# Optimization experiments

Hardware: AMD Instinct MI355X
Metric: run time of the kernel (lower is better)

## Reference

```python
import jax, jax.numpy as jnp
import numpy as np

BOUND = np.array([[-4.0, 4.0], [-4.0, 4.0], [-2.0, 2.0]], dtype=np.float32)
N_PTS = 1048576
PLANE_C = 3
PLANE_RES = [128, 256, 512, 1024]
N_LEVELS = 16
F_PER = 2
T = 2 ** 16  # hashmap size (log2_hashmap_size=16)
BASE_RES = 16
FINEST = int(float((BOUND[:, 1] - BOUND[:, 0]).max()) / 0.02)  # 400
_growth = np.exp(np.log(FINEST / BASE_RES) / (N_LEVELS - 1))
HASH_RES = np.floor(BASE_RES * _growth ** np.arange(N_LEVELS)).astype(np.float32)
PRIMES = jnp.array([1, 2654435761, 805459861], dtype=jnp.uint32)


def setup_inputs() -> dict:
    key = jax.random.key(0)
    ks = jax.random.split(key, 32)
    lo = jnp.asarray(BOUND[:, 0]); hi = jnp.asarray(BOUND[:, 1])
    inp = {}
    inp['p'] = jax.random.uniform(ks[0], (N_PTS, 3), dtype=jnp.float32) * (hi - lo) + lo
    i = 1
    for li, r in enumerate(PLANE_RES):
        for name in ('xy', 'xz', 'yz'):
            inp[f'plane_{name}_{li}'] = 0.1 * jax.random.normal(ks[i], (PLANE_C, r, r), dtype=jnp.float32)
            i += 1
    inp['hash_table'] = jax.random.uniform(ks[i], (N_LEVELS, T, F_PER), dtype=jnp.float32, minval=-1e-4, maxval=1e-4); i += 1

    def lin(k, fi, fo):
        s = 1.0 / np.sqrt(fi)
        k1, k2 = jax.random.split(k)
        return (jax.random.uniform(k1, (fi, fo), minval=-s, maxval=s, dtype=jnp.float32),
                jax.random.uniform(k2, (fo,), minval=-s, maxval=s, dtype=jnp.float32))

    c_in = 12 * PLANE_C + N_LEVELS * F_PER  # 68
    inp['W0'], inp['b0'] = lin(ks[i], c_in, 64); i += 1
    inp['W1'], inp['b1'] = lin(ks[i], 64, 64); i += 1
    inp['Wo'], inp['bo'] = lin(ks[i], 64, 33); i += 1  # 1 sdf + 32 geo_feat
    inp['Wc0'], inp['bc0'] = lin(ks[i], 12 * PLANE_C + 32, 64); i += 1
    inp['Wc1'], inp['bc1'] = lin(ks[i], 64, 32); i += 1
    inp['Wco'], inp['bco'] = lin(ks[i], 32, 3); i += 1
    return inp


def sample_plane(plane, u, v):
    """Bilinear grid_sample, align_corners=True, padding_mode='border'.
    plane: (C,H,W); u indexes W, v indexes H; u,v in [-1,1]. Returns (N,C)."""
    C, H, W = plane.shape
    x = jnp.clip((u + 1.0) * 0.5 * (W - 1), 0.0, W - 1)
    y = jnp.clip((v + 1.0) * 0.5 * (H - 1), 0.0, H - 1)
    x0 = jnp.floor(x); y0 = jnp.floor(y)
    wx = x - x0; wy = y - y0
    x0i = x0.astype(jnp.int32); y0i = y0.astype(jnp.int32)
    x1i = jnp.minimum(x0i + 1, W - 1); y1i = jnp.minimum(y0i + 1, H - 1)
    g = lambda yi, xi: plane[:, yi, xi]  # (C,N)
    out = (g(y0i, x0i) * ((1 - wy) * (1 - wx)) + g(y0i, x1i) * ((1 - wy) * wx)
           + g(y1i, x0i) * (wy * (1 - wx)) + g(y1i, x1i) * (wy * wx))
    return out.T


def hash_encode(p01, table):
    """Multi-res hash grid (instant-ngp style). p01: (N,3) in [0,1]; table: (L,T,F) -> (N, L*F)."""
    res = jnp.asarray(HASH_RES)  # (L,)

    def level(r, tab):
        x = p01 * r
        x0 = jnp.floor(x)
        w = x - x0
        xi = x0.astype(jnp.uint32)  # (N,3)
        feat = jnp.zeros((p01.shape[0], F_PER), dtype=table.dtype)
        for dz in (0, 1):
            for dy in (0, 1):
                for dx in (0, 1):
                    c = xi + jnp.array([dx, dy, dz], dtype=jnp.uint32)
                    h = c * PRIMES[None, :]
                    idx = ((h[:, 0] ^ h[:, 1] ^ h[:, 2]) % T).astype(jnp.int32)
                    wgt = ((w[:, 0] if dx else 1 - w[:, 0])
                           * (w[:, 1] if dy else 1 - w[:, 1])
                           * (w[:, 2] if dz else 1 - w[:, 2]))
                    feat = feat + tab[idx] * wgt[:, None]
        return feat  # (N,F)

    feats = jax.vmap(level, in_axes=(0, 0))(res, table)  # (L,N,F)
    return jnp.transpose(feats, (1, 0, 2)).reshape(p01.shape[0], N_LEVELS * F_PER)


def _forward(p, plane_xy_0, plane_xz_0, plane_yz_0, plane_xy_1, plane_xz_1, plane_yz_1,
             plane_xy_2, plane_xz_2, plane_yz_2, plane_xy_3, plane_xz_3, plane_yz_3,
             hash_table, W0, b0, W1, b1, Wo, bo, Wc0, bc0, Wc1, bc1, Wco, bco):
    bound = jnp.asarray(BOUND)
    p_nor = (p - bound[:, 0]) / (bound[:, 1] - bound[:, 0]) * 2.0 - 1.0  # normalize_3d_coordinate
    u, v, w = p_nor[:, 0], p_nor[:, 1], p_nor[:, 2]
    levels = [(plane_xy_0, plane_xz_0, plane_yz_0), (plane_xy_1, plane_xz_1, plane_yz_1),
              (plane_xy_2, plane_xz_2, plane_yz_2), (plane_xy_3, plane_xz_3, plane_yz_3)]
    feats = []
    for pxy, pxz, pyz in levels:
        feats += [sample_plane(pxy, u, v), sample_plane(pxz, u, w), sample_plane(pyz, v, w)]
    plane_feat = jnp.concatenate(feats, axis=-1)  # (N, 36)
    hfeat = hash_encode((p_nor + 1.0) * 0.5, hash_table)  # (N, 32)
    # SDF branch
    h = jnp.concatenate([plane_feat, hfeat], axis=-1)  # (N, 68)
    h = jax.nn.relu(h @ W0 + b0)
    h = jax.nn.relu(h @ W1 + b1)
    sf = jnp.tanh(h @ Wo + bo)
    sdf, geo_feat = sf[:, :1], sf[:, 1:]
    # RGB branch
    c = jnp.concatenate([geo_feat, plane_feat], axis=-1)  # (N, 68)
    c = jax.nn.relu(c @ Wc0 + bc0)
    c = jax.nn.relu(c @ Wc1 + bc1)
    rgb = jax.nn.sigmoid(c @ Wco + bco)
    return jnp.concatenate([rgb, sdf], axis=-1)  # (N, 4)


def reference(p, plane_xy_0, plane_xz_0, plane_yz_0, plane_xy_1, plane_xz_1, plane_yz_1,
              plane_xy_2, plane_xz_2, plane_yz_2, plane_xy_3, plane_xz_3, plane_yz_3,
              hash_table, W0, b0, W1, b1, Wo, bo, Wc0, bc0, Wc1, bc1, Wco, bco):
    return _forward(p, plane_xy_0, plane_xz_0, plane_yz_0, plane_xy_1, plane_xz_1, plane_yz_1,
                    plane_xy_2, plane_xz_2, plane_yz_2, plane_xy_3, plane_xz_3, plane_yz_3,
                    hash_table, W0, b0, W1, b1, Wo, bo, Wc0, bc0, Wc1, bc1, Wco, bco)
```

## Files before the change

kernel.cpp:

```cpp
#include <hip/hip_runtime.h>

#define NPTS 1048576
#define NBKT 262144

typedef short bhalf8 __attribute__((ext_vector_type(8)));
typedef _Float16 halfv8 __attribute__((ext_vector_type(8)));
typedef _Float16 halfv2 __attribute__((ext_vector_type(2)));
typedef float floatx4 __attribute__((ext_vector_type(4)));

#define WSZ 24320
#define MLP_THREADS 1024
#define MLP_WAVES 16

#define PB_PLANES 16320
#define PB_HASH 4096
#define PB_HIST 4096

__device__ const float HRg[16] = {16.f, 19.f, 24.f, 30.f, 37.f, 46.f, 57.f, 71.f,
                                  89.f, 110.f, 136.f, 169.f, 210.f, 260.f, 322.f, 400.f};


__device__ __forceinline__ float my_tanh(float x) {
  float e = __expf(2.f * x);
  return 1.f - 2.f * __builtin_amdgcn_rcpf(e + 1.f);
}

__device__ __forceinline__ float my_sigmoid(float x) {
  return __builtin_amdgcn_rcpf(1.f + __expf(-x));
}

__device__ __forceinline__ unsigned short f2h(float v) {
  _Float16 h = (_Float16)v;
  unsigned short u;
  __builtin_memcpy(&u, &h, 2);
  return u;
}

__device__ __forceinline__ float h2f(unsigned short u) {
  _Float16 h;
  __builtin_memcpy(&h, &u, 2);
  return (float)h;
}

__device__ __forceinline__ float texch(uint2 t, int c) {
  unsigned short u = (c == 0) ? (unsigned short)(t.x & 0xffffu)
                   : (c == 1) ? (unsigned short)(t.x >> 16)
                              : (unsigned short)(t.y & 0xffffu);
  return h2f(u);
}

__device__ __forceinline__ unsigned mort6(unsigned x) {
  return (x & 1) | ((x & 2) << 2) | ((x & 4) << 4) |
         ((x & 8) << 6) | ((x & 16) << 8) | ((x & 32) << 10);
}

__device__ __forceinline__ unsigned morton_key(float px, float py, float pz) {
  float qx = (px + 4.f) * 0.125f, qy = (py + 4.f) * 0.125f, qz = (pz + 2.f) * 0.25f;
  unsigned kx = min(63, max(0, (int)(qx * 64.f)));
  unsigned ky = min(63, max(0, (int)(qy * 64.f)));
  unsigned kz = min(63, max(0, (int)(qz * 64.f)));
  return mort6(kx) | (mort6(ky) << 1) | (mort6(kz) << 2);
}

__device__ __forceinline__ unsigned hash_level(const unsigned* __restrict__ ht, int lv,
                                               float q0, float q1, float q2) {
  const float r = HRg[lv];
  float x0 = q0 * r, x1 = q1 * r, x2 = q2 * r;
  float f0 = floorf(x0), f1 = floorf(x1), f2 = floorf(x2);
  float w0 = x0 - f0, w1 = x1 - f1, w2 = x2 - f2;
  unsigned i0 = (unsigned)(int)f0, i1 = (unsigned)(int)f1, i2 = (unsigned)(int)f2;
  const unsigned* __restrict__ hb = ht + ((unsigned)lv << 16);
  unsigned tv[8];
#pragma unroll
  for (int dz = 0; dz < 2; ++dz)
#pragma unroll
    for (int dy = 0; dy < 2; ++dy)
#pragma unroll
      for (int dx = 0; dx < 2; ++dx) {
        unsigned h = (i0 + dx) ^ ((i1 + dy) * 2654435761u) ^ ((i2 + dz) * 805459861u);
        tv[dz * 4 + dy * 2 + dx] = hb[h & 65535u];
      }
  halfv2 acc2 = {(_Float16)0.f, (_Float16)0.f};
#pragma unroll
  for (int c = 0; c < 8; ++c) {
    const int dx = c & 1, dy = (c >> 1) & 1, dz = c >> 2;
    float wgt = (dx ? w0 : 1.f - w0) * (dy ? w1 : 1.f - w1) * (dz ? w2 : 1.f - w2);
    halfv2 th;
    __builtin_memcpy(&th, &tv[c], 4);
    _Float16 wh = (_Float16)wgt;
    halfv2 w2v = {wh, wh};
    acc2 = th * w2v + acc2;
  }
  unsigned res;
  __builtin_memcpy(&res, &acc2, 4);
  return res;
}

__device__ __forceinline__ uint2 sampleP(const uint2* __restrict__ planes, int s,
                                         float u, float v, float w) {
  const int level = s / 3;
  const int m = s - level * 3;
  const float a = (m == 2) ? v : u;
  const float b = (m == 0) ? v : w;
  const int R = 128 << level;
  const unsigned base = 16384u * ((1u << (2 * level)) - 1u) + (unsigned)m * (unsigned)(R * R);
  const float Rm1 = (float)(R - 1);
  float x = fminf(fmaxf((a + 1.f) * 0.5f * Rm1, 0.f), Rm1);
  float y = fminf(fmaxf((b + 1.f) * 0.5f * Rm1, 0.f), Rm1);
  float x0f = floorf(x), y0f = floorf(y);
  float wx = x - x0f, wy = y - y0f;
  int x0 = (int)x0f, y0 = (int)y0f;
  int x1 = min(x0 + 1, R - 1), y1 = min(y0 + 1, R - 1);
  uint2 t00 = planes[base + y0 * R + x0];
  uint2 t01 = planes[base + y0 * R + x1];
  uint2 t10 = planes[base + y1 * R + x0];
  uint2 t11 = planes[base + y1 * R + x1];
  _Float16 h00 = (_Float16)((1.f - wy) * (1.f - wx));
  _Float16 h01 = (_Float16)((1.f - wy) * wx);
  _Float16 h10 = (_Float16)(wy * (1.f - wx));
  _Float16 h11 = (_Float16)(wy * wx);
  halfv2 w00 = {h00, h00}, w01 = {h01, h01}, w10 = {h10, h10}, w11 = {h11, h11};
  halfv2 l00, l01, l10, l11, u00, u01, u10, u11;
  __builtin_memcpy(&l00, &t00.x, 4); __builtin_memcpy(&u00, &t00.y, 4);
  __builtin_memcpy(&l01, &t01.x, 4); __builtin_memcpy(&u01, &t01.y, 4);
  __builtin_memcpy(&l10, &t10.x, 4); __builtin_memcpy(&u10, &t10.y, 4);
  __builtin_memcpy(&l11, &t11.x, 4); __builtin_memcpy(&u11, &t11.y, 4);
  halfv2 alo = l00 * w00 + l01 * w01 + l10 * w10 + l11 * w11;
  halfv2 ahi = u00 * w00 + u01 * w01 + u10 * w10 + u11 * w11;
  uint2 r;
  __builtin_memcpy(&r.x, &alo, 4);
  __builtin_memcpy(&r.y, &ahi, 4);
  return r;
}


struct PrepParams {
  const float* psrc[12];
  ushort4* pdst[12];
  const float* hash;
  unsigned* hashb;
  const float* p;
  unsigned* hist;
};

__global__ __launch_bounds__(256) void prep_kernel(PrepParams P) {
  const int b = blockIdx.x;
  if (b < PB_PLANES) {
    const int CUM[13] = {0, 16384, 32768, 49152, 114688, 180224, 245760,
                         507904, 770048, 1032192, 2080768, 3129344, 4177920};
    const int RESL[12] = {128, 128, 128, 256, 256, 256, 512, 512, 512, 1024, 1024, 1024};
    const int s = b << 8;
    int pi = 0;
#pragma unroll
    for (int i = 1; i < 12; ++i)
      if (s >= CUM[i]) pi = i;
    const int li = s + threadIdx.x - CUM[pi];
    const int R = RESL[pi];
    const int n = R * R;
    const float* __restrict__ src = P.psrc[pi];
    ushort4 t;
    t.x = f2h(src[li]);
    t.y = f2h(src[n + li]);
    t.z = f2h(src[2 * n + li]);
    t.w = 0;
    P.pdst[pi][li] = t;
  } else if (b < PB_PLANES + PB_HASH) {
    const int i = ((b - PB_PLANES) << 8) + threadIdx.x;
    float2 v = *(const float2*)(P.hash + (size_t)i * 2);
    P.hashb[i] = (unsigned)f2h(v.x) | ((unsigned)f2h(v.y) << 16);
  } else {
    const int i = ((b - PB_PLANES - PB_HASH) << 8) + threadIdx.x;
    const float* pp = P.p + (size_t)i * 3;
    unsigned k = morton_key(pp[0], pp[1], pp[2]);
    atomicAdd(&P.hist[k], 1u);
  }
}


__global__ __launch_bounds__(256) void scan1_kernel(const unsigned* __restrict__ hist,
                                                    unsigned* __restrict__ partial) {
  __shared__ unsigned s[256];
  const int b = blockIdx.x, t = threadIdx.x;
  uint4 v = ((const uint4*)(hist + b * 1024))[t];
  s[t] = v.x + v.y + v.z + v.w;
  __syncthreads();
  for (int d = 128; d > 0; d >>= 1) {
    if (t < d) s[t] += s[t + d];
    __syncthreads();
  }
  if (t == 0) partial[b] = s[0];
}

__global__ __launch_bounds__(256) void scan2_kernel(const unsigned* __restrict__ partial,
                                                    unsigned* __restrict__ base) {
  __shared__ unsigned s[256];
  const int t = threadIdx.x;
  s[t] = partial[t];
  __syncthreads();
  for (int d = 1; d < 256; d <<= 1) {
    unsigned v = (t >= d) ? s[t - d] : 0u;
    __syncthreads();
    s[t] += v;
    __syncthreads();
  }
  base[t] = (t == 0) ? 0u : s[t - 1];
}

__global__ __launch_bounds__(256) void scan3_kernel(const unsigned* __restrict__ hist,
                                                    const unsigned* __restrict__ base,
                                                    unsigned* __restrict__ cursor) {
  __shared__ unsigned s[256];
  const int b = blockIdx.x, t = threadIdx.x;
  uint4 v = ((const uint4*)(hist + b * 1024))[t];
  unsigned sum = v.x + v.y + v.z + v.w;
  s[t] = sum;
  __syncthreads();
  for (int d = 1; d < 256; d <<= 1) {
    unsigned x = (t >= d) ? s[t - d] : 0u;
    __syncthreads();
    s[t] += x;
    __syncthreads();
  }
  unsigned off = base[b] + s[t] - sum;
  uint4 c;
  c.x = off;
  c.y = off + v.x;
  c.z = off + v.x + v.y;
  c.w = off + v.x + v.y + v.z;
  ((uint4*)(cursor + b * 1024))[t] = c;
}

__global__ __launch_bounds__(256) void scatter_kernel(const float* __restrict__ p,
                                                      unsigned* __restrict__ cursor,
                                                      float4* __restrict__ qs) {
  int i = blockIdx.x * 256 + threadIdx.x;
  const float* pp = p + (size_t)i * 3;
  const float px = pp[0], py = pp[1], pz = pp[2];
  unsigned k = morton_key(px, py, pz);
  unsigned slot = atomicAdd(&cursor[k], 1u);
  float4 q;
  q.x = (px + 4.f) * 0.125f;
  q.y = (py + 4.f) * 0.125f;
  q.z = (pz + 2.f) * 0.25f;
  q.w = __uint_as_float((unsigned)i);
  qs[slot] = q;
}


__global__ __launch_bounds__(256) void repack_plane(const float* __restrict__ src,
                                                    ushort4* __restrict__ dst, int R) {
  int i = blockIdx.x * 256 + threadIdx.x;
  int n = R * R;
  if (i >= n) return;
  ushort4 t;
  t.x = f2h(src[i]);
  t.y = f2h(src[n + i]);
  t.z = f2h(src[2 * n + i]);
  t.w = 0;
  dst[i] = t;
}


__device__ __forceinline__ void sample3i(const uint2* __restrict__ pl,
                                         float a, float b, int R, float* f) {
  const float Rm1 = (float)(R - 1);
  float x = fminf(fmaxf((a + 1.f) * 0.5f * Rm1, 0.f), Rm1);
  float y = fminf(fmaxf((b + 1.f) * 0.5f * Rm1, 0.f), Rm1);
  float x0f = floorf(x), y0f = floorf(y);
  float wx = x - x0f, wy = y - y0f;
  int x0 = (int)x0f, y0 = (int)y0f;
  int x1 = min(x0 + 1, R - 1), y1 = min(y0 + 1, R - 1);
  float w00 = (1.f - wy) * (1.f - wx);
  float w01 = (1.f - wy) * wx;
  float w10 = wy * (1.f - wx);
  float w11 = wy * wx;
  uint2 t00 = pl[y0 * R + x0];
  uint2 t01 = pl[y0 * R + x1];
  uint2 t10 = pl[y1 * R + x0];
  uint2 t11 = pl[y1 * R + x1];
#pragma unroll
  for (int c = 0; c < 3; ++c) {
    f[c] = texch(t00, c) * w00 + texch(t01, c) * w01 +
           texch(t10, c) * w10 + texch(t11, c) * w11;
  }
}

__device__ __forceinline__ void sample3f(const float* __restrict__ pl,
                                         float a, float b, int R, float* f) {
  const float Rm1 = (float)(R - 1);
  float x = fminf(fmaxf((a + 1.f) * 0.5f * Rm1, 0.f), Rm1);
  float y = fminf(fmaxf((b + 1.f) * 0.5f * Rm1, 0.f), Rm1);
  float x0f = floorf(x), y0f = floorf(y);
  float wx = x - x0f, wy = y - y0f;
  int x0 = (int)x0f, y0 = (int)y0f;
  int x1 = min(x0 + 1, R - 1), y1 = min(y0 + 1, R - 1);
  float w00 = (1.f - wy) * (1.f - wx);
  float w01 = (1.f - wy) * wx;
  float w10 = wy * (1.f - wx);
  float w11 = wy * wx;
  int i00 = y0 * R + x0, i01 = y0 * R + x1;
  int i10 = y1 * R + x0, i11 = y1 * R + x1;
  const int R2 = R * R;
#pragma unroll
  for (int c = 0; c < 3; ++c) {
    const float* base = pl + c * R2;
    f[c] = base[i00] * w00 + base[i01] * w01 + base[i10] * w10 + base[i11] * w11;
  }
}


struct MlpWParams {
  const uint2* planes;
  const unsigned* hashb;
  const float4* qs;
  const float* W0; const float* b0;
  const float* W1; const float* b1;
  const float* Wo; const float* bo;
  const float* Wc0; const float* bc0;
  const float* Wc1; const float* bc1;
  const float* Wco; const float* bco;
  float* out;
};

template <int MODE>
__device__ __forceinline__ void stage_w(const float* __restrict__ src, int K, int Nsrc,
                                        int STR, int NPAD, int OFF, short* Wlds, int tid) {
  const int total = NPAD * STR;
  for (int idx = tid; idx < total; idx += MLP_THREADS) {
    int c = idx / STR;
    int kp = idx - c * STR;
    int sk = -1;
    if (MODE == 0) {
      if (kp < 48) {
        int s = kp >> 2, ch = kp & 3;
        if (ch < 3) sk = s * 3 + ch;
      } else if (kp < 80) {
        sk = 36 + (kp - 48);
      }
    } else if (MODE == 1) {
      if (kp < 32) {
        sk = kp;
      } else if (kp < 80) {
        int s = (kp - 32) >> 2, ch = (kp - 32) & 3;
        if (ch < 3) sk = 32 + s * 3 + ch;
      }
    } else {
      if (kp < K) sk = kp;
    }
    float val = (sk >= 0 && c < Nsrc) ? src[sk * Nsrc + c] : 0.f;
    Wlds[OFF + idx] = (short)f2h(val);
  }
}

__device__ __forceinline__ void stage_b(const float* __restrict__ src, int Nsrc, int NPAD,
                                        int BOFF, float* Blds, int tid) {
  for (int j = tid; j < NPAD; j += MLP_THREADS) Blds[BOFF + j] = (j < Nsrc) ? src[j] : 0.f;
}

__device__ __forceinline__ halfv8 as_h8(bhalf8 s) {
  halfv8 h;
  __builtin_memcpy(&h, &s, 16);
  return h;
}

__device__ __forceinline__ halfv8 frag4(unsigned d0, unsigned d1, unsigned d2, unsigned d3) {
  bhalf8 r;
  r[0] = (short)(d0 & 0xffffu); r[1] = (short)(d0 >> 16);
  r[2] = (short)(d1 & 0xffffu); r[3] = (short)(d1 >> 16);
  r[4] = (short)(d2 & 0xffffu); r[5] = (short)(d2 >> 16);
  r[6] = (short)(d3 & 0xffffu); r[7] = (short)(d3 >> 16);
  return as_h8(r);
}

__device__ __forceinline__ halfv8 ldS(const short* scr, int rowl, int grp, int s) {
  return *(const halfv8*)&scr[rowl * 72 + 32 * s + 8 * grp];
}

template <int NT, int KS, int OFF, int STR>
__device__ __forceinline__ void mlayer(const halfv8 (&af)[KS], floatx4 (&acc)[NT],
                                       const short* Wlds, int rowl, int grp) {
#pragma unroll
  for (int n = 0; n < NT; ++n) {
    floatx4 a{};
#pragma unroll
    for (int s = 0; s < KS; ++s) {
      const int wo = OFF + (16 * n + rowl) * STR + 32 * s + 8 * grp;
      const halfv8 wA = *(const halfv8*)&Wlds[wo];
      a = __builtin_amdgcn_mfma_f32_16x16x32_f16(wA, af[s], a, 0, 0, 0);
    }
    acc[n] = a;
  }
}

template <int NT>
__device__ __forceinline__ void relu_wr(const floatx4 (&acc)[NT], const float* Blds,
                                        int boff, short* scr, int rowl, int grp) {
#pragma unroll
  for (int n = 0; n < NT; ++n) {
    const int cbase = 16 * n + 4 * grp;
    short4 v4;
    float v0 = fmaxf(acc[n][0] + Blds[boff + cbase + 0], 0.f);
    float v1 = fmaxf(acc[n][1] + Blds[boff + cbase + 1], 0.f);
    float v2 = fmaxf(acc[n][2] + Blds[boff + cbase + 2], 0.f);
    float v3 = fmaxf(acc[n][3] + Blds[boff + cbase + 3], 0.f);
    v4.x = (short)f2h(v0);
    v4.y = (short)f2h(v1);
    v4.z = (short)f2h(v2);
    v4.w = (short)f2h(v3);
    *(short4*)&scr[rowl * 72 + cbase] = v4;
  }
}

__device__ __forceinline__ void tanh_wr(const floatx4 (&acc)[3], const float* Blds,
                                        short* scr, float* ost, int rowl, int grp) {
#pragma unroll
  for (int n = 0; n < 3; ++n) {
#pragma unroll
    for (int r = 0; r < 4; ++r) {
      const int c = 16 * n + 4 * grp + r;
      float v = my_tanh(acc[n][r] + Blds[128 + c]);
      if (c == 0) ost[rowl * 4 + 3] = v;
      if (c >= 1 && c <= 32) scr[rowl * 72 + c - 1] = (short)f2h(v);
    }
  }
}

__global__ __launch_bounds__(MLP_THREADS) void mlp_fused(MlpWParams P) {
  __shared__ short Wlds[WSZ];
  __shared__ float Blds[288];
  __shared__ short Scr[MLP_WAVES * 16 * 72];
  __shared__ float Ost[MLP_WAVES][16][4];

  const int tid = threadIdx.x;

  stage_w<0>(P.W0,  96, 64, 104, 64,     0, Wlds, tid);
  stage_w<2>(P.W1,  64, 64,  72, 64,  6656, Wlds, tid);
  stage_w<2>(P.Wo,  64, 33,  72, 48, 11264, Wlds, tid);
  stage_w<1>(P.Wc0, 96, 64, 104, 64, 14720, Wlds, tid);
  stage_w<2>(P.Wc1, 64, 32,  72, 32, 21376, Wlds, tid);
  stage_w<2>(P.Wco, 32,  3,  40, 16, 23680, Wlds, tid);
  stage_b(P.b0,  64, 64,   0, Blds, tid);
  stage_b(P.b1,  64, 64,  64, Blds, tid);
  stage_b(P.bo,  33, 48, 128, Blds, tid);
  stage_b(P.bc0, 64, 64, 176, Blds, tid);
  stage_b(P.bc1, 32, 32, 240, Blds, tid);
  stage_b(P.bco,  3, 16, 272, Blds, tid);
  __syncthreads();

  const int wave = tid >> 6, lane = tid & 63;
  const int rowl = lane & 15, grp = lane >> 4;
  short* scr0 = &Scr[wave * 16 * 72];
  float* ost0 = &Ost[wave][0][0];

  int bid = blockIdx.x;
  bid = (bid & 7) * 64 + (bid >> 3);

  for (int t = 0; t < 8; ++t) {
    const int wbase = ((bid * 8 + t) * MLP_WAVES + wave) * 16;
    const int pt = wbase + rowl;

    float4 q4 = P.qs[pt];
    const float q0 = q4.x, q1 = q4.y, q2 = q4.z;
    const unsigned pid = __float_as_uint(q4.w);
    const float u = 2.f * q0 - 1.f;
    const float v = 2.f * q1 - 1.f;
    const float w = 2.f * q2 - 1.f;

    uint2 sA = sampleP(P.planes, 2 * grp, u, v, w);
    uint2 sB = sampleP(P.planes, 2 * grp + 1, u, v, w);
    uint2 sC = {0u, 0u}, sD = {0u, 0u};
    if (grp < 2) {
      sC = sampleP(P.planes, 8 + 2 * grp, u, v, w);
      sD = sampleP(P.planes, 9 + 2 * grp, u, v, w);
    }
    const int lbase = (grp < 2) ? (8 + 4 * grp) : (4 * grp - 8);
    unsigned h0 = hash_level(P.hashb, lbase + 0, q0, q1, q2);
    unsigned h1 = hash_level(P.hashb, lbase + 1, q0, q1, q2);
    unsigned h2 = hash_level(P.hashb, lbase + 2, q0, q1, q2);
    unsigned h3 = hash_level(P.hashb, lbase + 3, q0, q1, q2);

    halfv8 af0 = frag4(sA.x, sA.y, sB.x, sB.y);
    halfv8 af1 = (grp < 2) ? frag4(sC.x, sC.y, sD.x, sD.y) : frag4(h0, h1, h2, h3);
    halfv8 af2 = (grp < 2) ? frag4(h0, h1, h2, h3) : frag4(0u, 0u, 0u, 0u);
    halfv8 zf = frag4(0u, 0u, 0u, 0u);

    {
      halfv8 afA[3] = {af0, af1, af2};
      floatx4 accA[4];
      mlayer<4, 3, 0, 104>(afA, accA, Wlds, rowl, grp);
      relu_wr<4>(accA, Blds, 0, scr0, rowl, grp);
    }
    {
      halfv8 afA[2] = {ldS(scr0, rowl, grp, 0), ldS(scr0, rowl, grp, 1)};
      floatx4 accA[4];
      mlayer<4, 2, 6656, 72>(afA, accA, Wlds, rowl, grp);
      relu_wr<4>(accA, Blds, 64, scr0, rowl, grp);
    }
    {
      halfv8 afA[2] = {ldS(scr0, rowl, grp, 0), ldS(scr0, rowl, grp, 1)};
      floatx4 accA[3];
      mlayer<3, 2, 11264, 72>(afA, accA, Wlds, rowl, grp);
      tanh_wr(accA, Blds, scr0, ost0, rowl, grp);
    }
    {
      halfv8 afA[3] = {ldS(scr0, rowl, grp, 0), af0, (grp < 2) ? af1 : zf};
      floatx4 accA[4];
      mlayer<4, 3, 14720, 104>(afA, accA, Wlds, rowl, grp);
      relu_wr<4>(accA, Blds, 176, scr0, rowl, grp);
    }
    {
      halfv8 afA[2] = {ldS(scr0, rowl, grp, 0), ldS(scr0, rowl, grp, 1)};
      floatx4 accA[2];
      mlayer<2, 2, 21376, 72>(afA, accA, Wlds, rowl, grp);
      relu_wr<2>(accA, Blds, 240, scr0, rowl, grp);
    }
    {
      halfv8 afA[1] = {ldS(scr0, rowl, grp, 0)};
      floatx4 accA[1];
      mlayer<1, 1, 23680, 40>(afA, accA, Wlds, rowl, grp);
#pragma unroll
      for (int r = 0; r < 4; ++r) {
        const int c = 4 * grp + r;
        if (c < 3) {
          float vA = my_sigmoid(accA[0][r] + Blds[272 + c]);
          ost0[rowl * 4 + c] = vA;
        }
      }
    }

    if (lane < 16) {
      float4 o = *(float4*)&Ost[wave][lane][0];
      ((float4*)P.out)[pid] = o;
    }
  }
}


struct DecParams {
  const float* p;
  const float* pl[12];
  const uint2* pli[12];
  const float* hash;
  const float* W0; const float* b0;
  const float* W1; const float* b1;
  const float* Wo; const float* bo;
  const float* Wc0; const float* bc0;
  const float* Wc1; const float* bc1;
  const float* Wco; const float* bco;
  float* out;
};

template <bool ILV>
__global__ __launch_bounds__(256) void dec_kernel(DecParams P) {
  const int tid = blockIdx.x * 256 + threadIdx.x;

  const float* __restrict__ pp = P.p + (size_t)tid * 3;
  const float px = pp[0], py = pp[1], pz = pp[2];

  const float u = (px + 4.f) * 0.25f - 1.f;
  const float v = (py + 4.f) * 0.25f - 1.f;
  const float w = (pz + 2.f) * 0.5f - 1.f;

  float feat[68];
  {
    const int RES[4] = {128, 256, 512, 1024};
#pragma unroll
    for (int li = 0; li < 4; ++li) {
      if (ILV) {
        sample3i(P.pli[li * 3 + 0], u, v, RES[li], &feat[li * 9 + 0]);
        sample3i(P.pli[li * 3 + 1], u, w, RES[li], &feat[li * 9 + 3]);
        sample3i(P.pli[li * 3 + 2], v, w, RES[li], &feat[li * 9 + 6]);
      } else {
        sample3f(P.pl[li * 3 + 0], u, v, RES[li], &feat[li * 9 + 0]);
        sample3f(P.pl[li * 3 + 1], u, w, RES[li], &feat[li * 9 + 3]);
        sample3f(P.pl[li * 3 + 2], v, w, RES[li], &feat[li * 9 + 6]);
      }
    }
  }

  {
    const float q0 = (px + 4.f) * 0.125f;
    const float q1 = (py + 4.f) * 0.125f;
    const float q2 = (pz + 2.f) * 0.25f;
    const float* __restrict__ ht = P.hash;
#pragma unroll
    for (int l = 0; l < 16; ++l) {
      const float r = HRg[l];
      float x0 = q0 * r, x1 = q1 * r, x2 = q2 * r;
      float f0 = floorf(x0), f1 = floorf(x1), f2 = floorf(x2);
      float w0 = x0 - f0, w1 = x1 - f1, w2 = x2 - f2;
      unsigned i0 = (unsigned)(int)f0, i1 = (unsigned)(int)f1, i2 = (unsigned)(int)f2;
      float a0 = 0.f, a1 = 0.f;
#pragma unroll
      for (int dz = 0; dz < 2; ++dz)
#pragma unroll
        for (int dy = 0; dy < 2; ++dy)
#pragma unroll
          for (int dx = 0; dx < 2; ++dx) {
            unsigned h = (i0 + dx) ^ ((i1 + dy) * 2654435761u) ^ ((i2 + dz) * 805459861u);
            unsigned idx = h & 65535u;
            const float2 tv = *(const float2*)(ht + (((unsigned)l << 16) + idx) * 2);
            float wgt = (dx ? w0 : 1.f - w0) * (dy ? w1 : 1.f - w1) * (dz ? w2 : 1.f - w2);
            a0 = fmaf(tv.x, wgt, a0);
            a1 = fmaf(tv.y, wgt, a1);
          }
      feat[36 + l * 2] = a0;
      feat[36 + l * 2 + 1] = a1;
    }
  }

  float acc[64];
#pragma unroll
  for (int j = 0; j < 64; ++j) acc[j] = P.b0[j];
#pragma unroll
  for (int i = 0; i < 68; ++i) {
    const float a = feat[i];
    const float* wr = P.W0 + i * 64;
#pragma unroll
    for (int j = 0; j < 64; ++j) acc[j] = fmaf(a, wr[j], acc[j]);
  }
  float hid[64];
#pragma unroll
  for (int j = 0; j < 64; ++j) hid[j] = fmaxf(acc[j], 0.f);

#pragma unroll
  for (int j = 0; j < 64; ++j) acc[j] = P.b1[j];
#pragma unroll
  for (int i = 0; i < 64; ++i) {
    const float a = hid[i];
    const float* wr = P.W1 + i * 64;
#pragma unroll
    for (int j = 0; j < 64; ++j) acc[j] = fmaf(a, wr[j], acc[j]);
  }
#pragma unroll
  for (int j = 0; j < 64; ++j) hid[j] = fmaxf(acc[j], 0.f);

  float so[33];
#pragma unroll
  for (int j = 0; j < 33; ++j) so[j] = P.bo[j];
#pragma unroll
  for (int i = 0; i < 64; ++i) {
    const float a = hid[i];
    const float* wr = P.Wo + i * 33;
#pragma unroll
    for (int j = 0; j < 33; ++j) so[j] = fmaf(a, wr[j], so[j]);
  }
  const float sdf = my_tanh(so[0]);
  float geo[32];
#pragma unroll
  for (int j = 0; j < 32; ++j) geo[j] = my_tanh(so[j + 1]);

#pragma unroll
  for (int j = 0; j < 64; ++j) acc[j] = P.bc0[j];
#pragma unroll
  for (int i = 0; i < 32; ++i) {
    const float a = geo[i];
    const float* wr = P.Wc0 + i * 64;
#pragma unroll
    for (int j = 0; j < 64; ++j) acc[j] = fmaf(a, wr[j], acc[j]);
  }
#pragma unroll
  for (int i = 0; i < 36; ++i) {
    const float a = feat[i];
    const float* wr = P.Wc0 + (32 + i) * 64;
#pragma unroll
    for (int j = 0; j < 64; ++j) acc[j] = fmaf(a, wr[j], acc[j]);
  }
#pragma unroll
  for (int j = 0; j < 64; ++j) hid[j] = fmaxf(acc[j], 0.f);

  float c1[32];
#pragma unroll
  for (int j = 0; j < 32; ++j) c1[j] = P.bc1[j];
#pragma unroll
  for (int i = 0; i < 64; ++i) {
    const float a = hid[i];
    const float* wr = P.Wc1 + i * 32;
#pragma unroll
    for (int j = 0; j < 32; ++j) c1[j] = fmaf(a, wr[j], c1[j]);
  }

  float r0 = P.bco[0], r1 = P.bco[1], r2 = P.bco[2];
#pragma unroll
  for (int i = 0; i < 32; ++i) {
    const float a = fmaxf(c1[i], 0.f);
    r0 = fmaf(a, P.Wco[i * 3 + 0], r0);
    r1 = fmaf(a, P.Wco[i * 3 + 1], r1);
    r2 = fmaf(a, P.Wco[i * 3 + 2], r2);
  }

  float4 o;
  o.x = my_sigmoid(r0);
  o.y = my_sigmoid(r1);
  o.z = my_sigmoid(r2);
  o.w = sdf;
  ((float4*)P.out)[tid] = o;
}


extern "C" void kernel_launch(void* const* d_in, const int* in_sizes, int n_in,
                              void* d_out, int out_size, void* d_ws, size_t ws_size,
                              hipStream_t stream) {
  const int RES[4] = {128, 256, 512, 1024};
  const size_t planes_bytes = (size_t)4177920 * 8;
  const size_t hash_bytes = (size_t)16 * 65536 * 4;
  const size_t qs_bytes = (size_t)NPTS * 16;
  const size_t hist_bytes = (size_t)NBKT * 4;
  const size_t need_fused = planes_bytes + hash_bytes + qs_bytes + 2 * hist_bytes + 4096;
  const size_t need_mid = planes_bytes + 64;

  char* wsp = (char*)d_ws;
  const float* p = (const float*)d_in[0];

  if (ws_size >= need_fused) {
    size_t off = 0;
    PrepParams PP;
    PP.p = p;
    PP.hash = (const float*)d_in[13];
    const uint2* planes = (const uint2*)wsp;
    for (int i = 0; i < 12; ++i) {
      int R = RES[i / 3];
      PP.psrc[i] = (const float*)d_in[1 + i];
      PP.pdst[i] = (ushort4*)(wsp + off);
      off += (size_t)R * R * 8;
    }
    unsigned* hashb = (unsigned*)(wsp + off);
    PP.hashb = hashb;
    off += hash_bytes;
    float4* qs = (float4*)(wsp + off);
    off += qs_bytes;
    unsigned* hist = (unsigned*)(wsp + off);
    off += hist_bytes;
    unsigned* cursor = (unsigned*)(wsp + off);
    off += hist_bytes;
    unsigned* partial = (unsigned*)(wsp + off);
    off += 1024;
    unsigned* base = (unsigned*)(wsp + off);
    off += 1024;
    PP.hist = hist;

    hipMemsetAsync(hist, 0, hist_bytes, stream);
    prep_kernel<<<PB_PLANES + PB_HASH + PB_HIST, 256, 0, stream>>>(PP);
    scan1_kernel<<<256, 256, 0, stream>>>(hist, partial);
    scan2_kernel<<<1, 256, 0, stream>>>(partial, base);
    scan3_kernel<<<256, 256, 0, stream>>>(hist, base, cursor);
    scatter_kernel<<<NPTS / 256, 256, 0, stream>>>(p, cursor, qs);

    MlpWParams MP;
    MP.planes = planes;
    MP.hashb = hashb;
    MP.qs = qs;
    MP.W0 = (const float*)d_in[14]; MP.b0 = (const float*)d_in[15];
    MP.W1 = (const float*)d_in[16]; MP.b1 = (const float*)d_in[17];
    MP.Wo = (const float*)d_in[18]; MP.bo = (const float*)d_in[19];
    MP.Wc0 = (const float*)d_in[20]; MP.bc0 = (const float*)d_in[21];
    MP.Wc1 = (const float*)d_in[22]; MP.bc1 = (const float*)d_in[23];
    MP.Wco = (const float*)d_in[24]; MP.bco = (const float*)d_in[25];
    MP.out = (float*)d_out;
    mlp_fused<<<512, MLP_THREADS, 0, stream>>>(MP);
    return;
  }

  DecParams P;
  P.p = p;
  for (int i = 0; i < 12; ++i) P.pl[i] = (const float*)d_in[1 + i];
  P.hash = (const float*)d_in[13];
  P.W0  = (const float*)d_in[14]; P.b0  = (const float*)d_in[15];
  P.W1  = (const float*)d_in[16]; P.b1  = (const float*)d_in[17];
  P.Wo  = (const float*)d_in[18]; P.bo  = (const float*)d_in[19];
  P.Wc0 = (const float*)d_in[20]; P.bc0 = (const float*)d_in[21];
  P.Wc1 = (const float*)d_in[22]; P.bc1 = (const float*)d_in[23];
  P.Wco = (const float*)d_in[24]; P.bco = (const float*)d_in[25];
  P.out = (float*)d_out;

  if (ws_size >= need_mid) {
    size_t off = 0;
    for (int i = 0; i < 12; ++i) {
      int R = RES[i / 3];
      int n = R * R;
      P.pli[i] = (const uint2*)(wsp + off);
      repack_plane<<<(n + 255) / 256, 256, 0, stream>>>(
          (const float*)d_in[1 + i], (ushort4*)(wsp + off), R);
      off += (size_t)n * 8;
    }
    dec_kernel<true><<<NPTS / 256, 256, 0, stream>>>(P);
  } else {
    for (int i = 0; i < 12; ++i) P.pli[i] = nullptr;
    dec_kernel<false><<<NPTS / 256, 256, 0, stream>>>(P);
  }
}
```

Measured before the change: 418.8 us.

## Software-pipeline plane and hash gathers across tiles in fused MLP kernel

Splits the plane sampling and hash encoding into an issue phase (raw gathers) and a finish phase (interpolation), and double-buffers them. The gathers for the next 16-point tile are issued while the current tile runs its MFMA layers, hiding gather latency. Blocks shrink to 512 threads with launch bounds allowing 2 blocks per CU and twice as many blocks, and the LDS scratch row stride is padded from 72 to 80 shorts, presumably to reduce bank conflicts. The cost is many more live registers for the raw gather buffers (two Raw structs), which could lower occupancy or cause spills.

```diff
diff --git a/kernel.cpp b/kernel.cpp
--- a/kernel.cpp
+++ b/kernel.cpp
@@ -9,8 +9,10 @@
 typedef float floatx4 __attribute__((ext_vector_type(4)));
 
 #define WSZ 24320
-#define MLP_THREADS 1024
-#define MLP_WAVES 16
+#define MLP_THREADS 512
+#define MLP_WAVES 8
+#define MLP_BLOCKS 1024
+#define SCR_STR 80
 
 #define PB_PLANES 16320
 #define PB_HASH 4096
@@ -62,59 +64,46 @@
   return mort6(kx) | (mort6(ky) << 1) | (mort6(kz) << 2);
 }
 
-__device__ __forceinline__ unsigned hash_level(const unsigned* __restrict__ ht, int lv,
-                                               float q0, float q1, float q2) {
-  const float r = HRg[lv];
-  float x0 = q0 * r, x1 = q1 * r, x2 = q2 * r;
-  float f0 = floorf(x0), f1 = floorf(x1), f2 = floorf(x2);
-  float w0 = x0 - f0, w1 = x1 - f1, w2 = x2 - f2;
-  unsigned i0 = (unsigned)(int)f0, i1 = (unsigned)(int)f1, i2 = (unsigned)(int)f2;
-  const unsigned* __restrict__ hb = ht + ((unsigned)lv << 16);
-  unsigned tv[8];
-#pragma unroll
-  for (int dz = 0; dz < 2; ++dz)
-#pragma unroll
-    for (int dy = 0; dy < 2; ++dy)
-#pragma unroll
-      for (int dx = 0; dx < 2; ++dx) {
-        unsigned h = (i0 + dx) ^ ((i1 + dy) * 2654435761u) ^ ((i2 + dz) * 805459861u);
-        tv[dz * 4 + dy * 2 + dx] = hb[h & 65535u];
-      }
-  halfv2 acc2 = {(_Float16)0.f, (_Float16)0.f};
-#pragma unroll
-  for (int c = 0; c < 8; ++c) {
-    const int dx = c & 1, dy = (c >> 1) & 1, dz = c >> 2;
-    float wgt = (dx ? w0 : 1.f - w0) * (dy ? w1 : 1.f - w1) * (dz ? w2 : 1.f - w2);
-    halfv2 th;
-    __builtin_memcpy(&th, &tv[c], 4);
-    _Float16 wh = (_Float16)wgt;
-    halfv2 w2v = {wh, wh};
-    acc2 = th * w2v + acc2;
-  }
-  unsigned res;
-  __builtin_memcpy(&res, &acc2, 4);
-  return res;
-}
-
-__device__ __forceinline__ uint2 sampleP(const uint2* __restrict__ planes, int s,
-                                         float u, float v, float w) {
-  const int level = s / 3;
-  const int m = s - level * 3;
+
+struct Raw {
+  uint2 a00, a01, a10, a11;
+  uint2 b00, b01, b10, b11;
+  uint2 c00, c01, c10, c11;
+  uint2 d00, d01, d10, d11;
+  unsigned tv0[8], tv1[8], tv2[8], tv3[8];
+};
+
+__device__ __forceinline__ void plane_const(int s, int& R, int& m, unsigned& base) {
+  int level = s / 3;
+  m = s - 3 * level;
+  R = 128 << level;
+  base = 16384u * ((1u << (2 * level)) - 1u) + (unsigned)m * (unsigned)(R * R);
+}
+
+__device__ __forceinline__ void plane_iss(const uint2* __restrict__ planes, int R,
+                                          unsigned base, int m, float u, float v, float w,
+                                          uint2& t00, uint2& t01, uint2& t10, uint2& t11) {
   const float a = (m == 2) ? v : u;
   const float b = (m == 0) ? v : w;
-  const int R = 128 << level;
-  const unsigned base = 16384u * ((1u << (2 * level)) - 1u) + (unsigned)m * (unsigned)(R * R);
   const float Rm1 = (float)(R - 1);
   float x = fminf(fmaxf((a + 1.f) * 0.5f * Rm1, 0.f), Rm1);
   float y = fminf(fmaxf((b + 1.f) * 0.5f * Rm1, 0.f), Rm1);
-  float x0f = floorf(x), y0f = floorf(y);
-  float wx = x - x0f, wy = y - y0f;
-  int x0 = (int)x0f, y0 = (int)y0f;
+  int x0 = (int)x, y0 = (int)y;
   int x1 = min(x0 + 1, R - 1), y1 = min(y0 + 1, R - 1);
-  uint2 t00 = planes[base + y0 * R + x0];
-  uint2 t01 = planes[base + y0 * R + x1];
-  uint2 t10 = planes[base + y1 * R + x0];
-  uint2 t11 = planes[base + y1 * R + x1];
+  t00 = planes[base + y0 * R + x0];
+  t01 = planes[base + y0 * R + x1];
+  t10 = planes[base + y1 * R + x0];
+  t11 = planes[base + y1 * R + x1];
+}
+
+__device__ __forceinline__ uint2 plane_fin(int R, int m, float u, float v, float w,
+                                           uint2 t00, uint2 t01, uint2 t10, uint2 t11) {
+  const float a = (m == 2) ? v : u;
+  const float b = (m == 0) ? v : w;
+  const float Rm1 = (float)(R - 1);
+  float x = fminf(fmaxf((a + 1.f) * 0.5f * Rm1, 0.f), Rm1);
+  float y = fminf(fmaxf((b + 1.f) * 0.5f * Rm1, 0.f), Rm1);
+  float wx = x - floorf(x), wy = y - floorf(y);
   _Float16 h00 = (_Float16)((1.f - wy) * (1.f - wx));
   _Float16 h01 = (_Float16)((1.f - wy) * wx);
   _Float16 h10 = (_Float16)(wy * (1.f - wx));
@@ -131,6 +120,43 @@
   __builtin_memcpy(&r.x, &alo, 4);
   __builtin_memcpy(&r.y, &ahi, 4);
   return r;
+}
+
+__device__ __forceinline__ void hash_iss(const unsigned* __restrict__ hb, float r,
+                                         float q0, float q1, float q2, unsigned (&tv)[8]) {
+  float x0 = q0 * r, x1 = q1 * r, x2 = q2 * r;
+  unsigned i0 = (unsigned)(int)floorf(x0);
+  unsigned i1 = (unsigned)(int)floorf(x1);
+  unsigned i2 = (unsigned)(int)floorf(x2);
+#pragma unroll
+  for (int dz = 0; dz < 2; ++dz)
+#pragma unroll
+    for (int dy = 0; dy < 2; ++dy)
+#pragma unroll
+      for (int dx = 0; dx < 2; ++dx) {
+        unsigned h = (i0 + dx) ^ ((i1 + dy) * 2654435761u) ^ ((i2 + dz) * 805459861u);
+        tv[dz * 4 + dy * 2 + dx] = hb[h & 65535u];
+      }
+}
+
+__device__ __forceinline__ unsigned hash_fin(float r, float q0, float q1, float q2,
+                                             const unsigned (&tv)[8]) {
+  float x0 = q0 * r, x1 = q1 * r, x2 = q2 * r;
+  float w0 = x0 - floorf(x0), w1 = x1 - floorf(x1), w2 = x2 - floorf(x2);
+  halfv2 acc2 = {(_Float16)0.f, (_Float16)0.f};
+#pragma unroll
+  for (int c = 0; c < 8; ++c) {
+    const int dx = c & 1, dy = (c >> 1) & 1, dz = c >> 2;
+    float wgt = (dx ? w0 : 1.f - w0) * (dy ? w1 : 1.f - w1) * (dz ? w2 : 1.f - w2);
+    halfv2 th;
+    __builtin_memcpy(&th, &tv[c], 4);
+    _Float16 wh = (_Float16)wgt;
+    halfv2 w2v = {wh, wh};
+    acc2 = th * w2v + acc2;
+  }
+  unsigned res;
+  __builtin_memcpy(&res, &acc2, 4);
+  return res;
 }
 
 
@@ -373,7 +399,7 @@
 }
 
 __device__ __forceinline__ halfv8 ldS(const short* scr, int rowl, int grp, int s) {
-  return *(const halfv8*)&scr[rowl * 72 + 32 * s + 8 * grp];
+  return *(const halfv8*)&scr[rowl * SCR_STR + 32 * s + 8 * grp];
 }
 
 template <int NT, int KS, int OFF, int STR>
@@ -407,7 +433,7 @@
     v4.y = (short)f2h(v1);
     v4.z = (short)f2h(v2);
     v4.w = (short)f2h(v3);
-    *(short4*)&scr[rowl * 72 + cbase] = v4;
+    *(short4*)&scr[rowl * SCR_STR + cbase] = v4;
   }
 }
 
@@ -420,15 +446,15 @@
       const int c = 16 * n + 4 * grp + r;
       float v = my_tanh(acc[n][r] + Blds[128 + c]);
       if (c == 0) ost[rowl * 4 + 3] = v;
-      if (c >= 1 && c <= 32) scr[rowl * 72 + c - 1] = (short)f2h(v);
-    }
-  }
-}
-
-__global__ __launch_bounds__(MLP_THREADS) void mlp_fused(MlpWParams P) {
+      if (c >= 1 && c <= 32) scr[rowl * SCR_STR + c - 1] = (short)f2h(v);
+    }
+  }
+}
+
+__global__ __launch_bounds__(MLP_THREADS, 2) void mlp_fused(MlpWParams P) {
   __shared__ short Wlds[WSZ];
   __shared__ float Blds[288];
-  __shared__ short Scr[MLP_WAVES * 16 * 72];
+  __shared__ short Scr[MLP_WAVES * 16 * SCR_STR];
   __shared__ float Ost[MLP_WAVES][16][4];
 
   const int tid = threadIdx.x;
@@ -449,40 +475,67 @@
 
   const int wave = tid >> 6, lane = tid & 63;
   const int rowl = lane & 15, grp = lane >> 4;
-  short* scr0 = &Scr[wave * 16 * 72];
+  short* scr0 = &Scr[wave * 16 * SCR_STR];
   float* ost0 = &Ost[wave][0][0];
 
   int bid = blockIdx.x;
-  bid = (bid & 7) * 64 + (bid >> 3);
-
-  for (int t = 0; t < 8; ++t) {
-    const int wbase = ((bid * 8 + t) * MLP_WAVES + wave) * 16;
-    const int pt = wbase + rowl;
-
-    float4 q4 = P.qs[pt];
+  bid = (bid & 7) * (MLP_BLOCKS / 8) + (bid >> 3);
+
+  const int s0 = 2 * grp, s1 = 2 * grp + 1;
+  const int s2 = 8 + 2 * grp, s3 = 9 + 2 * grp;
+  int R0, m0, R1, m1, R2, m2, R3, m3;
+  unsigned B0, B1, B2, B3;
+  plane_const(s0, R0, m0, B0);
+  plane_const(s1, R1, m1, B1);
+  plane_const(s2, R2, m2, B2);
+  plane_const(s3, R3, m3, B3);
+  const int lbase = (grp < 2) ? (8 + 4 * grp) : (4 * grp - 8);
+  const unsigned* hb0 = P.hashb + ((unsigned)(lbase + 0) << 16);
+  const unsigned* hb1 = P.hashb + ((unsigned)(lbase + 1) << 16);
+  const unsigned* hb2 = P.hashb + ((unsigned)(lbase + 2) << 16);
+  const unsigned* hb3 = P.hashb + ((unsigned)(lbase + 3) << 16);
+  const float hr0 = HRg[lbase + 0], hr1 = HRg[lbase + 1];
+  const float hr2 = HRg[lbase + 2], hr3 = HRg[lbase + 3];
+
+  auto issue = [&](const float4& q4, Raw& r) {
     const float q0 = q4.x, q1 = q4.y, q2 = q4.z;
-    const unsigned pid = __float_as_uint(q4.w);
-    const float u = 2.f * q0 - 1.f;
-    const float v = 2.f * q1 - 1.f;
-    const float w = 2.f * q2 - 1.f;
-
-    uint2 sA = sampleP(P.planes, 2 * grp, u, v, w);
-    uint2 sB = sampleP(P.planes, 2 * grp + 1, u, v, w);
+    const float uu = 2.f * q0 - 1.f, vv = 2.f * q1 - 1.f, ww = 2.f * q2 - 1.f;
+    plane_iss(P.planes, R0, B0, m0, uu, vv, ww, r.a00, r.a01, r.a10, r.a11);
+    plane_iss(P.planes, R1, B1, m1, uu, vv, ww, r.b00, r.b01, r.b10, r.b11);
+    if (grp < 2) {
+      plane_iss(P.planes, R2, B2, m2, uu, vv, ww, r.c00, r.c01, r.c10, r.c11);
+      plane_iss(P.planes, R3, B3, m3, uu, vv, ww, r.d00, r.d01, r.d10, r.d11);
+    }
+    hash_iss(hb0, hr0, q0, q1, q2, r.tv0);
+    hash_iss(hb1, hr1, q0, q1, q2, r.tv1);
+    hash_iss(hb2, hr2, q0, q1, q2, r.tv2);
+    hash_iss(hb3, hr3, q0, q1, q2, r.tv3);
+  };
+
+  auto body = [&](int t, Raw& cur, Raw& nxt, const float4& qcur, float4& qnxt) {
+    if (t < 7) qnxt = P.qs[((bid * 8 + (t + 1)) * MLP_WAVES + wave) * 16 + rowl];
+
+    const float q0 = qcur.x, q1 = qcur.y, q2 = qcur.z;
+    const unsigned pid = __float_as_uint(qcur.w);
+    const float uu = 2.f * q0 - 1.f, vv = 2.f * q1 - 1.f, ww = 2.f * q2 - 1.f;
+    uint2 sA = plane_fin(R0, m0, uu, vv, ww, cur.a00, cur.a01, cur.a10, cur.a11);
+    uint2 sB = plane_fin(R1, m1, uu, vv, ww, cur.b00, cur.b01, cur.b10, cur.b11);
     uint2 sC = {0u, 0u}, sD = {0u, 0u};
     if (grp < 2) {
-      sC = sampleP(P.planes, 8 + 2 * grp, u, v, w);
-      sD = sampleP(P.planes, 9 + 2 * grp, u, v, w);
-    }
-    const int lbase = (grp < 2) ? (8 + 4 * grp) : (4 * grp - 8);
-    unsigned h0 = hash_level(P.hashb, lbase + 0, q0, q1, q2);
-    unsigned h1 = hash_level(P.hashb, lbase + 1, q0, q1, q2);
-    unsigned h2 = hash_level(P.hashb, lbase + 2, q0, q1, q2);
-    unsigned h3 = hash_level(P.hashb, lbase + 3, q0, q1, q2);
+      sC = plane_fin(R2, m2, uu, vv, ww, cur.c00, cur.c01, cur.c10, cur.c11);
+      sD = plane_fin(R3, m3, uu, vv, ww, cur.d00, cur.d01, cur.d10, cur.d11);
+    }
+    unsigned h0 = hash_fin(hr0, q0, q1, q2, cur.tv0);
+    unsigned h1 = hash_fin(hr1, q0, q1, q2, cur.tv1);
+    unsigned h2 = hash_fin(hr2, q0, q1, q2, cur.tv2);
+    unsigned h3 = hash_fin(hr3, q0, q1, q2, cur.tv3);
 
     halfv8 af0 = frag4(sA.x, sA.y, sB.x, sB.y);
     halfv8 af1 = (grp < 2) ? frag4(sC.x, sC.y, sD.x, sD.y) : frag4(h0, h1, h2, h3);
     halfv8 af2 = (grp < 2) ? frag4(h0, h1, h2, h3) : frag4(0u, 0u, 0u, 0u);
     halfv8 zf = frag4(0u, 0u, 0u, 0u);
+
+    if (t < 7) issue(qnxt, nxt);
 
     {
       halfv8 afA[3] = {af0, af1, af2};
@@ -532,6 +585,16 @@
       float4 o = *(float4*)&Ost[wave][lane][0];
       ((float4*)P.out)[pid] = o;
     }
+  };
+
+  Raw rA, rB;
+  float4 qA, qB;
+  qA = P.qs[((bid * 8 + 0) * MLP_WAVES + wave) * 16 + rowl];
+  issue(qA, rA);
+
+  for (int tt = 0; tt < 4; ++tt) {
+    body(2 * tt, rA, rB, qA, qB);
+    body(2 * tt + 1, rB, rA, qB, qA);
   }
 }
 
@@ -757,7 +820,7 @@
     MP.Wc1 = (const float*)d_in[22]; MP.bc1 = (const float*)d_in[23];
     MP.Wco = (const float*)d_in[24]; MP.bco = (const float*)d_in[25];
     MP.out = (float*)d_out;
-    mlp_fused<<<512, MLP_THREADS, 0, stream>>>(MP);
+    mlp_fused<<<MLP_BLOCKS, MLP_THREADS, 0, stream>>>(MP);
     return;
   }
 
```

Result: slower. 432.2 us (+3.2%).
